# Optimization experiments

Measured on AMD Instinct MI355X. Metric: run time of the kernel, lower is better.

## Reference

```python
import jax, jax.numpy as jnp
import numpy as np

N = 100000
E = 1200000
D = 64  # in_dim == out_dim


def leaky_relu(x, slope=0.2):
    return jnp.where(x >= 0, x, slope * x)


def setup_inputs() -> dict:
    key = jax.random.key(0)
    ks = jax.random.split(key, 10)
    indices = jax.random.randint(ks[0], (2, E), 0, N, dtype=jnp.int64)
    features = jax.random.normal(ks[1], (N, D), dtype=jnp.float32)
    e_r = jax.random.normal(ks[2], (E, D), dtype=jnp.float32)
    s = 1.0 / np.sqrt(D)
    W1_w = jax.random.normal(ks[3], (D, D), dtype=jnp.float32) * s
    W1_b = jax.random.normal(ks[4], (D,), dtype=jnp.float32) * s
    W2_w = jax.random.normal(ks[5], (D, D), dtype=jnp.float32) * s
    W2_b = jax.random.normal(ks[6], (D,), dtype=jnp.float32) * s
    Watt_w = jax.random.normal(ks[7], (D, D), dtype=jnp.float32) * s
    Watt_b = jax.random.normal(ks[8], (D,), dtype=jnp.float32) * s
    return {"indices": indices, "features": features, "e_r": e_r, "num_nodes": N,
            "W1_w": W1_w, "W1_b": W1_b, "W2_w": W2_w, "W2_b": W2_b,
            "Watt_w": Watt_w, "Watt_b": Watt_b}


def reference(indices, features, e_r, num_nodes, W1_w, W1_b, W2_w, W2_b, Watt_w, Watt_b):
    src, dst = indices[0], indices[1]
    out_dim = Watt_w.shape[0]

    # edge attention scores
    h_trans = features @ Watt_w.T + Watt_b          # (N, D)
    h_src = h_trans[src]                            # (E, D) gather
    h_dst = h_trans[dst]                            # (E, D) gather
    # e_r already aligned to out_dim (d_r == out_dim here)
    e_raw = jnp.sum(h_dst * jnp.tanh(h_src + e_r), axis=-1, keepdims=True)  # (E, 1)
    scaling = 1.0 / (out_dim ** 0.5)
    e_ij = leaky_relu(e_raw * scaling).astype(jnp.float32)

    # segment softmax over edges grouped by dst (max detached, as in original)
    max_score = jax.ops.segment_max(jax.lax.stop_gradient(e_ij), dst,
                                    num_segments=num_nodes)               # (N, 1)
    exp_e = jnp.exp(e_ij - max_score[dst])                                 # (E, 1)
    denom = jax.ops.segment_sum(exp_e, dst, num_segments=num_nodes)       # (N, 1)
    alpha = exp_e / (denom[dst] + 1e-9)                                    # (E, 1)

    # weighted scatter aggregation
    weighted_msg = features[src] * alpha.astype(features.dtype)            # (E, D)
    h_neigh = jax.ops.segment_sum(weighted_msg, dst, num_segments=num_nodes)  # (N, D)

    sum_h = features + h_neigh
    prod_h = features * h_neigh
    h_out = leaky_relu(sum_h @ W1_w.T + W1_b + (prod_h @ W2_w.T + W2_b))
    return h_out
```

## Files before the change

kernel.cpp:

```cpp
#include <hip/hip_runtime.h>
#include <hip/hip_bf16.h>

#define D 64
#define SCAN_CHUNK 2048

__device__ __forceinline__ float fast_tanh(float x) {
    float e2 = __expf(2.0f * x);
    return 1.0f - 2.0f / (e2 + 1.0f);
}

__device__ __forceinline__ float leaky(float x) {
    return x >= 0.0f ? x : 0.2f * x;
}

__global__ __launch_bounds__(256) void k_htrans(const float* __restrict__ feat,
                                                const float* __restrict__ W,
                                                const float* __restrict__ bias,
                                                float* __restrict__ out, int N)
{
    __shared__ float Wt[D][D];
    __shared__ float bsh[D];
    __shared__ float fs[32][D + 1];
    const int t = threadIdx.x;
    for (int i = t; i < D * D; i += 256) { Wt[i & 63][i >> 6] = W[i]; }
    if (t < D) bsh[t] = bias[t];
    const int cg = t & 15;
    const int rp = t >> 4;
    for (int g = 0; g < 2; ++g) {
        const int base = blockIdx.x * 64 + g * 32;
        __syncthreads();
        for (int i = t; i < 32 * D; i += 256) {
            int r = i >> 6, d = i & 63;
            int n = base + r;
            fs[r][d] = (n < N) ? feat[(size_t)n * D + d] : 0.0f;
        }
        __syncthreads();
        float4 acc0 = {0, 0, 0, 0}, acc1 = {0, 0, 0, 0};
        const int r0 = rp * 2, r1 = r0 + 1;
        #pragma unroll 8
        for (int d = 0; d < D; ++d) {
            const float4 w = *reinterpret_cast<const float4*>(&Wt[d][cg * 4]);
            const float f0 = fs[r0][d], f1 = fs[r1][d];
            acc0.x += f0 * w.x; acc0.y += f0 * w.y; acc0.z += f0 * w.z; acc0.w += f0 * w.w;
            acc1.x += f1 * w.x; acc1.y += f1 * w.y; acc1.z += f1 * w.z; acc1.w += f1 * w.w;
        }
        const float4 b4 = *reinterpret_cast<const float4*>(&bsh[cg * 4]);
        const int n0 = base + r0, n1 = base + r1;
        if (n0 < N) {
            float4 o = {acc0.x + b4.x, acc0.y + b4.y, acc0.z + b4.z, acc0.w + b4.w};
            *reinterpret_cast<float4*>(&out[(size_t)n0 * D + cg * 4]) = o;
        }
        if (n1 < N) {
            float4 o = {acc1.x + b4.x, acc1.y + b4.y, acc1.z + b4.z, acc1.w + b4.w};
            *reinterpret_cast<float4*>(&out[(size_t)n1 * D + cg * 4]) = o;
        }
    }
}

__global__ __launch_bounds__(256) void k_hist(const int* __restrict__ dst, int* __restrict__ cnt, int E)
{
    int e = blockIdx.x * 256 + threadIdx.x;
    if (e < E) atomicAdd(&cnt[dst[e]], 1);
}

__global__ __launch_bounds__(256) void k_scan1(int* __restrict__ offs, int* __restrict__ partials, int N)
{
    __shared__ int lds[256];
    const int t = threadIdx.x;
    const int base = blockIdx.x * SCAN_CHUNK + t * 8;
    int v[8];
    #pragma unroll
    for (int i = 0; i < 8; ++i) v[i] = (base + i < N) ? offs[base + i] : 0;
    int tot = 0;
    #pragma unroll
    for (int i = 0; i < 8; ++i) { int x = v[i]; v[i] = tot; tot += x; }
    lds[t] = tot;
    __syncthreads();
    for (int off = 1; off < 256; off <<= 1) {
        int x = 0;
        if (t >= off) x = lds[t - off];
        __syncthreads();
        lds[t] += x;
        __syncthreads();
    }
    const int texc = (t == 0) ? 0 : lds[t - 1];
    #pragma unroll
    for (int i = 0; i < 8; ++i)
        if (base + i < N) offs[base + i] = v[i] + texc;
    if (t == 255) partials[blockIdx.x] = lds[255];
}

__global__ void k_scan2(int* __restrict__ partials, int NB)
{
    if (threadIdx.x == 0 && blockIdx.x == 0) {
        int run = 0;
        for (int i = 0; i < NB; ++i) { int x = partials[i]; partials[i] = run; run += x; }
    }
}

__global__ __launch_bounds__(256) void k_scan3(int* __restrict__ offs, const int* __restrict__ partials, int N)
{
    const int add = partials[blockIdx.x];
    if (add == 0) return;
    const int base = blockIdx.x * SCAN_CHUNK + threadIdx.x * 8;
    #pragma unroll
    for (int i = 0; i < 8; ++i)
        if (base + i < N) offs[base + i] += add;
}

__global__ __launch_bounds__(256) void k_scatter(const int* __restrict__ dst,
                                                 const int* __restrict__ srcA,
                                                 int* __restrict__ offs,
                                                 int2* __restrict__ es, int E)
{
    int e = blockIdx.x * 256 + threadIdx.x;
    if (e < E) {
        int pos = atomicAdd(&offs[dst[e]], 1);
        es[pos] = make_int2(e, srcA[e]);
    }
}

__global__ __launch_bounds__(256) void k_fused(const int2* __restrict__ es,
                                               const int* __restrict__ offs,
                                               const float* __restrict__ ht,
                                               const float* __restrict__ er,
                                               const float* __restrict__ feat,
                                               float* __restrict__ hneigh, int N)
{
    const int t = threadIdx.x;
    const int lane = t & 63;
    const int n = blockIdx.x * 4 + (t >> 6);
    if (n >= N) return;
    const int sg = lane >> 4;
    const int dl = lane & 15;
    const int beg = (n == 0) ? 0 : offs[n - 1];
    const int end = offs[n];
    const float4 hd = *reinterpret_cast<const float4*>(ht + (size_t)n * D + dl * 4);
    float4 acc = {0, 0, 0, 0};
    float den = 0.0f;
    int p = beg + sg;
    int2 cur = make_int2(0, 0);
    if (p < end) cur = es[p];
    while (p < end) {
        const int pn = p + 4;
        int2 nxt = make_int2(0, 0);
        if (pn < end) nxt = es[pn];
        const float4 ev = *reinterpret_cast<const float4*>(er + (size_t)cur.x * D + dl * 4);
        const float4 hs = *reinterpret_cast<const float4*>(ht + (size_t)cur.y * D + dl * 4);
        const float4 f  = *reinterpret_cast<const float4*>(feat + (size_t)cur.y * D + dl * 4);
        float pp = hd.x * fast_tanh(hs.x + ev.x)
                 + hd.y * fast_tanh(hs.y + ev.y)
                 + hd.z * fast_tanh(hs.z + ev.z)
                 + hd.w * fast_tanh(hs.w + ev.w);
        pp += __shfl_xor(pp, 1);
        pp += __shfl_xor(pp, 2);
        pp += __shfl_xor(pp, 4);
        pp += __shfl_xor(pp, 8);
        const float ex = __expf(leaky(pp * 0.125f));
        den += ex;
        acc.x += ex * f.x; acc.y += ex * f.y; acc.z += ex * f.z; acc.w += ex * f.w;
        cur = nxt;
        p = pn;
    }
    den += __shfl_xor(den, 16);
    den += __shfl_xor(den, 32);
    acc.x += __shfl_xor(acc.x, 16); acc.x += __shfl_xor(acc.x, 32);
    acc.y += __shfl_xor(acc.y, 16); acc.y += __shfl_xor(acc.y, 32);
    acc.z += __shfl_xor(acc.z, 16); acc.z += __shfl_xor(acc.z, 32);
    acc.w += __shfl_xor(acc.w, 16); acc.w += __shfl_xor(acc.w, 32);
    if (sg == 0) {
        const float r = __builtin_amdgcn_rcpf(den + 1e-9f);
        float4 o = {acc.x * r, acc.y * r, acc.z * r, acc.w * r};
        *reinterpret_cast<float4*>(hneigh + (size_t)n * D + dl * 4) = o;
    }
}

__global__ __launch_bounds__(256) void k_out(const float* __restrict__ feat,
                                             const float* __restrict__ hneigh,
                                             const float* __restrict__ W1,
                                             const float* __restrict__ b1,
                                             const float* __restrict__ W2,
                                             const float* __restrict__ b2,
                                             float* __restrict__ out, int N)
{
    __shared__ float W1t[D][D];
    __shared__ float W2t[D][D];
    __shared__ float bsum[D];
    __shared__ float ss[32][D + 1];
    __shared__ float pp[32][D + 1];
    const int t = threadIdx.x;
    for (int i = t; i < D * D; i += 256) {
        W1t[i & 63][i >> 6] = W1[i];
        W2t[i & 63][i >> 6] = W2[i];
    }
    if (t < D) bsum[t] = b1[t] + b2[t];
    const int cg = t & 15;
    const int rp = t >> 4;
    for (int g = 0; g < 2; ++g) {
        const int base = blockIdx.x * 64 + g * 32;
        __syncthreads();
        for (int i = t; i < 32 * D; i += 256) {
            int r = i >> 6, d = i & 63;
            int n = base + r;
            float f = 0.0f, hn = 0.0f;
            if (n < N) { f = feat[(size_t)n * D + d]; hn = hneigh[(size_t)n * D + d]; }
            ss[r][d] = f + hn;
            pp[r][d] = f * hn;
        }
        __syncthreads();
        float4 a0 = {0, 0, 0, 0}, a1 = {0, 0, 0, 0};
        const int r0 = rp * 2, r1 = r0 + 1;
        #pragma unroll 4
        for (int d = 0; d < D; ++d) {
            const float4 w1 = *reinterpret_cast<const float4*>(&W1t[d][cg * 4]);
            const float4 w2 = *reinterpret_cast<const float4*>(&W2t[d][cg * 4]);
            const float s0 = ss[r0][d], p0 = pp[r0][d];
            const float s1 = ss[r1][d], p1 = pp[r1][d];
            a0.x += s0 * w1.x + p0 * w2.x; a0.y += s0 * w1.y + p0 * w2.y;
            a0.z += s0 * w1.z + p0 * w2.z; a0.w += s0 * w1.w + p0 * w2.w;
            a1.x += s1 * w1.x + p1 * w2.x; a1.y += s1 * w1.y + p1 * w2.y;
            a1.z += s1 * w1.z + p1 * w2.z; a1.w += s1 * w1.w + p1 * w2.w;
        }
        const float4 b4 = *reinterpret_cast<const float4*>(&bsum[cg * 4]);
        const int n0 = base + r0, n1 = base + r1;
        if (n0 < N) {
            float4 o = {leaky(a0.x + b4.x), leaky(a0.y + b4.y), leaky(a0.z + b4.z), leaky(a0.w + b4.w)};
            *reinterpret_cast<float4*>(&out[(size_t)n0 * D + cg * 4]) = o;
        }
        if (n1 < N) {
            float4 o = {leaky(a1.x + b4.x), leaky(a1.y + b4.y), leaky(a1.z + b4.z), leaky(a1.w + b4.w)};
            *reinterpret_cast<float4*>(&out[(size_t)n1 * D + cg * 4]) = o;
        }
    }
}

extern "C" void kernel_launch(void* const* d_in, const int* in_sizes, int n_in,
                              void* d_out, int out_size, void* d_ws, size_t ws_size,
                              hipStream_t stream) {
    const int*   idx  = (const int*)d_in[0];
    const float* feat = (const float*)d_in[1];
    const float* er   = (const float*)d_in[2];
    const float* W1   = (const float*)d_in[4];
    const float* b1   = (const float*)d_in[5];
    const float* W2   = (const float*)d_in[6];
    const float* b2   = (const float*)d_in[7];
    const float* Wa   = (const float*)d_in[8];
    const float* ba   = (const float*)d_in[9];

    const int E = in_sizes[0] / 2;
    const int N = in_sizes[1] / D;
    const int* srcI = idx;
    const int* dstI = idx + E;

    float* htrans = (float*)d_out;
    float* hneigh   = (float*)d_ws;
    int*   offs     = (int*)(hneigh + (size_t)N * D);
    int*   partials = offs + N;
    int2*  es       = (int2*)(partials + 256);

    const int NB = (N + SCAN_CHUNK - 1) / SCAN_CHUNK;

    hipMemsetAsync(offs, 0, (size_t)N * sizeof(int), stream);

    dim3 blk(256);
    k_htrans <<<dim3((N + 63) / 64), blk, 0, stream>>>(feat, Wa, ba, htrans, N);
    k_hist   <<<dim3((E + 255) / 256), blk, 0, stream>>>(dstI, offs, E);
    k_scan1  <<<dim3(NB), blk, 0, stream>>>(offs, partials, N);
    k_scan2  <<<dim3(1), dim3(64), 0, stream>>>(partials, NB);
    k_scan3  <<<dim3(NB), blk, 0, stream>>>(offs, partials, N);
    k_scatter<<<dim3((E + 255) / 256), blk, 0, stream>>>(dstI, srcI, offs, es, E);
    k_fused  <<<dim3((N + 3) / 4), blk, 0, stream>>>(es, offs, htrans, er, feat, hneigh, N);
    k_out    <<<dim3((N + 63) / 64), blk, 0, stream>>>(feat, hneigh, W1, b1, W2, b2, (float*)d_out, N);
}
```

Before: 729.9 us.

## Store h_trans and gathered features as bf16 and widen per-lane edge work

```diff
diff --git a/kernel.cpp b/kernel.cpp
--- a/kernel.cpp
+++ b/kernel.cpp
@@ -3,6 +3,9 @@
 
 #define D 64
 #define SCAN_CHUNK 2048
+
+typedef unsigned int uint_t;
+typedef unsigned short ushort_t;
 
 __device__ __forceinline__ float fast_tanh(float x) {
     float e2 = __expf(2.0f * x);
@@ -13,10 +16,25 @@
     return x >= 0.0f ? x : 0.2f * x;
 }
 
+__device__ __forceinline__ ushort_t f2bf(float x) {
+    uint_t u = __float_as_uint(x);
+    u += 0x7FFFu + ((u >> 16) & 1u);
+    return (ushort_t)(u >> 16);
+}
+__device__ __forceinline__ uint_t pack2bf(float lo, float hi) {
+    return (uint_t)f2bf(lo) | ((uint_t)f2bf(hi) << 16);
+}
+__device__ __forceinline__ void bf8_unpack(uint4 u, float* f) {
+    f[0] = __uint_as_float(u.x << 16); f[1] = __uint_as_float(u.x & 0xFFFF0000u);
+    f[2] = __uint_as_float(u.y << 16); f[3] = __uint_as_float(u.y & 0xFFFF0000u);
+    f[4] = __uint_as_float(u.z << 16); f[5] = __uint_as_float(u.z & 0xFFFF0000u);
+    f[6] = __uint_as_float(u.w << 16); f[7] = __uint_as_float(u.w & 0xFFFF0000u);
+}
+
 __global__ __launch_bounds__(256) void k_htrans(const float* __restrict__ feat,
                                                 const float* __restrict__ W,
                                                 const float* __restrict__ bias,
-                                                float* __restrict__ out, int N)
+                                                ushort_t* __restrict__ outB, int N)
 {
     __shared__ float Wt[D][D];
     __shared__ float bsh[D];
@@ -47,14 +65,27 @@
         const float4 b4 = *reinterpret_cast<const float4*>(&bsh[cg * 4]);
         const int n0 = base + r0, n1 = base + r1;
         if (n0 < N) {
-            float4 o = {acc0.x + b4.x, acc0.y + b4.y, acc0.z + b4.z, acc0.w + b4.w};
-            *reinterpret_cast<float4*>(&out[(size_t)n0 * D + cg * 4]) = o;
+            uint2 o = {pack2bf(acc0.x + b4.x, acc0.y + b4.y), pack2bf(acc0.z + b4.z, acc0.w + b4.w)};
+            *reinterpret_cast<uint2*>(&outB[(size_t)n0 * D + cg * 4]) = o;
         }
         if (n1 < N) {
-            float4 o = {acc1.x + b4.x, acc1.y + b4.y, acc1.z + b4.z, acc1.w + b4.w};
-            *reinterpret_cast<float4*>(&out[(size_t)n1 * D + cg * 4]) = o;
-        }
-    }
+            uint2 o = {pack2bf(acc1.x + b4.x, acc1.y + b4.y), pack2bf(acc1.z + b4.z, acc1.w + b4.w)};
+            *reinterpret_cast<uint2*>(&outB[(size_t)n1 * D + cg * 4]) = o;
+        }
+    }
+}
+
+__global__ __launch_bounds__(256) void k_tobf(const float* __restrict__ in,
+                                              ushort_t* __restrict__ out, int n8)
+{
+    int i = blockIdx.x * 256 + threadIdx.x;
+    if (i >= n8) return;
+    const float4 a = reinterpret_cast<const float4*>(in)[2 * i];
+    const float4 b = reinterpret_cast<const float4*>(in)[2 * i + 1];
+    uint4 o;
+    o.x = pack2bf(a.x, a.y); o.y = pack2bf(a.z, a.w);
+    o.z = pack2bf(b.x, b.y); o.w = pack2bf(b.z, b.w);
+    reinterpret_cast<uint4*>(out)[i] = o;
 }
 
 __global__ __launch_bounds__(256) void k_hist(const int* __restrict__ dst, int* __restrict__ cnt, int E)
@@ -122,56 +153,65 @@
 
 __global__ __launch_bounds__(256) void k_fused(const int2* __restrict__ es,
                                                const int* __restrict__ offs,
-                                               const float* __restrict__ ht,
+                                               const ushort_t* __restrict__ htB,
                                                const float* __restrict__ er,
-                                               const float* __restrict__ feat,
+                                               const ushort_t* __restrict__ featB,
                                                float* __restrict__ hneigh, int N)
 {
     const int t = threadIdx.x;
     const int lane = t & 63;
     const int n = blockIdx.x * 4 + (t >> 6);
     if (n >= N) return;
-    const int sg = lane >> 4;
-    const int dl = lane & 15;
+    const int sg = lane >> 3;
+    const int dl = lane & 7;
     const int beg = (n == 0) ? 0 : offs[n - 1];
     const int end = offs[n];
-    const float4 hd = *reinterpret_cast<const float4*>(ht + (size_t)n * D + dl * 4);
-    float4 acc = {0, 0, 0, 0};
+    float hd[8];
+    bf8_unpack(*reinterpret_cast<const uint4*>(htB + (size_t)n * D + dl * 8), hd);
+    float acc[8] = {0, 0, 0, 0, 0, 0, 0, 0};
     float den = 0.0f;
     int p = beg + sg;
     int2 cur = make_int2(0, 0);
     if (p < end) cur = es[p];
     while (p < end) {
-        const int pn = p + 4;
+        const int pn = p + 8;
         int2 nxt = make_int2(0, 0);
         if (pn < end) nxt = es[pn];
-        const float4 ev = *reinterpret_cast<const float4*>(er + (size_t)cur.x * D + dl * 4);
-        const float4 hs = *reinterpret_cast<const float4*>(ht + (size_t)cur.y * D + dl * 4);
-        const float4 f  = *reinterpret_cast<const float4*>(feat + (size_t)cur.y * D + dl * 4);
-        float pp = hd.x * fast_tanh(hs.x + ev.x)
-                 + hd.y * fast_tanh(hs.y + ev.y)
-                 + hd.z * fast_tanh(hs.z + ev.z)
-                 + hd.w * fast_tanh(hs.w + ev.w);
-        pp += __shfl_xor(pp, 1);
-        pp += __shfl_xor(pp, 2);
-        pp += __shfl_xor(pp, 4);
-        pp += __shfl_xor(pp, 8);
-        const float ex = __expf(leaky(pp * 0.125f));
+        float hs[8], f[8];
+        bf8_unpack(*reinterpret_cast<const uint4*>(htB + (size_t)cur.y * D + dl * 8), hs);
+        bf8_unpack(*reinterpret_cast<const uint4*>(featB + (size_t)cur.y * D + dl * 8), f);
+        const float4 e0 = *reinterpret_cast<const float4*>(er + (size_t)cur.x * D + dl * 8);
+        const float4 e1 = *reinterpret_cast<const float4*>(er + (size_t)cur.x * D + dl * 8 + 4);
+        float s = hd[0] * fast_tanh(hs[0] + e0.x)
+                + hd[1] * fast_tanh(hs[1] + e0.y)
+                + hd[2] * fast_tanh(hs[2] + e0.z)
+                + hd[3] * fast_tanh(hs[3] + e0.w)
+                + hd[4] * fast_tanh(hs[4] + e1.x)
+                + hd[5] * fast_tanh(hs[5] + e1.y)
+                + hd[6] * fast_tanh(hs[6] + e1.z)
+                + hd[7] * fast_tanh(hs[7] + e1.w);
+        s += __shfl_xor(s, 1);
+        s += __shfl_xor(s, 2);
+        s += __shfl_xor(s, 4);
+        const float ex = __expf(leaky(s * 0.125f));
         den += ex;
-        acc.x += ex * f.x; acc.y += ex * f.y; acc.z += ex * f.z; acc.w += ex * f.w;
+        #pragma unroll
+        for (int j = 0; j < 8; ++j) acc[j] += ex * f[j];
         cur = nxt;
         p = pn;
     }
-    den += __shfl_xor(den, 16);
-    den += __shfl_xor(den, 32);
-    acc.x += __shfl_xor(acc.x, 16); acc.x += __shfl_xor(acc.x, 32);
-    acc.y += __shfl_xor(acc.y, 16); acc.y += __shfl_xor(acc.y, 32);
-    acc.z += __shfl_xor(acc.z, 16); acc.z += __shfl_xor(acc.z, 32);
-    acc.w += __shfl_xor(acc.w, 16); acc.w += __shfl_xor(acc.w, 32);
+    #pragma unroll
+    for (int m = 8; m <= 32; m <<= 1) {
+        den += __shfl_xor(den, m);
+        #pragma unroll
+        for (int j = 0; j < 8; ++j) acc[j] += __shfl_xor(acc[j], m);
+    }
     if (sg == 0) {
         const float r = __builtin_amdgcn_rcpf(den + 1e-9f);
-        float4 o = {acc.x * r, acc.y * r, acc.z * r, acc.w * r};
-        *reinterpret_cast<float4*>(hneigh + (size_t)n * D + dl * 4) = o;
+        float4 o0 = {acc[0] * r, acc[1] * r, acc[2] * r, acc[3] * r};
+        float4 o1 = {acc[4] * r, acc[5] * r, acc[6] * r, acc[7] * r};
+        *reinterpret_cast<float4*>(hneigh + (size_t)n * D + dl * 8) = o0;
+        *reinterpret_cast<float4*>(hneigh + (size_t)n * D + dl * 8 + 4) = o1;
     }
 }
 
@@ -252,23 +292,25 @@
     const int* srcI = idx;
     const int* dstI = idx + E;
 
-    float* htrans = (float*)d_out;
-    float* hneigh   = (float*)d_ws;
-    int*   offs     = (int*)(hneigh + (size_t)N * D);
-    int*   partials = offs + N;
-    int2*  es       = (int2*)(partials + 256);
+    float*    hneigh   = (float*)d_ws;
+    ushort_t* htB      = (ushort_t*)(hneigh + (size_t)N * D);
+    ushort_t* featB    = htB + (size_t)N * D;
+    int2*     es       = (int2*)(featB + (size_t)N * D);
+    int*      offs     = (int*)(es + E);
+    int*      partials = offs + N;
 
     const int NB = (N + SCAN_CHUNK - 1) / SCAN_CHUNK;
 
     hipMemsetAsync(offs, 0, (size_t)N * sizeof(int), stream);
 
     dim3 blk(256);
-    k_htrans <<<dim3((N + 63) / 64), blk, 0, stream>>>(feat, Wa, ba, htrans, N);
+    k_htrans <<<dim3((N + 63) / 64), blk, 0, stream>>>(feat, Wa, ba, htB, N);
+    k_tobf   <<<dim3((N * D / 8 + 255) / 256), blk, 0, stream>>>(feat, featB, N * D / 8);
     k_hist   <<<dim3((E + 255) / 256), blk, 0, stream>>>(dstI, offs, E);
     k_scan1  <<<dim3(NB), blk, 0, stream>>>(offs, partials, N);
     k_scan2  <<<dim3(1), dim3(64), 0, stream>>>(partials, NB);
     k_scan3  <<<dim3(NB), blk, 0, stream>>>(offs, partials, N);
     k_scatter<<<dim3((E + 255) / 256), blk, 0, stream>>>(dstI, srcI, offs, es, E);
-    k_fused  <<<dim3((N + 3) / 4), blk, 0, stream>>>(es, offs, htrans, er, feat, hneigh, N);
+    k_fused  <<<dim3((N + 3) / 4), blk, 0, stream>>>(es, offs, htB, er, featB, hneigh, N);
     k_out    <<<dim3((N + 63) / 64), blk, 0, stream>>>(feat, hneigh, W1, b1, W2, b2, (float*)d_out, N);
 }
```

Result: no change. 717.3 us (-1.7%).
